# Kernel tuning notes

Hardware: AMD Instinct MI355X
Metric: run time of the kernel (lower is better)

## Reference

```python
import jax, jax.numpy as jnp
import numpy as np
from jax import lax

EPS = 1e-5

def conv2d(x, w, groups=1, pad=0):
    return lax.conv_general_dilated(
        x, w, window_strides=(1, 1), padding=[(pad, pad), (pad, pad)],
        dimension_numbers=('NCHW', 'OIHW', 'NCHW'), feature_group_count=groups)

def setup_inputs() -> dict:
    key = jax.random.key(0)
    ks = jax.random.split(key, 10)
    B, C, H, W = 8, 64, 128, 128
    s = 0.05
    f32 = jnp.float32
    return {
        'x': jax.random.normal(ks[0], (B, C, H, W), f32),
        # key_embed: Conv2d(64,64,3,groups=8,bias=False) -> weight [64, 64/8, 3, 3]
        'w_key': jax.random.normal(ks[1], (64, 8, 3, 3), f32) * s,
        # embed[0]: Conv2d(128,32,1,groups=2,bias=False) -> [32, 128/2, 1, 1]
        'w_e1': jax.random.normal(ks[2], (32, 64, 1, 1), f32) * s,
        # embed[2]: Conv2d(32,72,1,groups=2,bias=True) -> [72, 32/2, 1, 1]
        'w_e2': jax.random.normal(ks[3], (72, 16, 1, 1), f32) * s,
        'b_e2': jax.random.normal(ks[4], (72,), f32) * s,
        # GroupNorm(num_groups=8, num_channels=72) affine params
        'gn_w': jnp.ones((72,), f32),
        'gn_b': jnp.zeros((72,), f32),
        # conv1x1: Conv2d(64,64,1,groups=2,bias=False) -> [64, 32, 1, 1]
        'w_c1': jax.random.normal(ks[5], (64, 32, 1, 1), f32) * s,
        # conv_du: Conv2d(64,4,1,bias=False), Conv2d(4,64,1,bias=False)
        'w_du1': jax.random.normal(ks[6], (4, 64, 1, 1), f32) * s,
        'w_du2': jax.random.normal(ks[7], (64, 4, 1, 1), f32) * s,
    }

def reference(x, w_key, w_e1, w_e2, b_e2, gn_w, gn_b, w_c1, w_du1, w_du2):
    B, C, H, W = x.shape  # C == 64
    KK = 9                # kernel_size^2
    # key embedding: grouped 3x3 conv + ReLU
    k = jax.nn.relu(conv2d(x, w_key, groups=8, pad=1))
    # interleave x and k along channels: view of [B,64,2,H,W] -> [B,128,H,W]
    qk = jnp.stack([x, k], axis=2).reshape(B, 2 * C, H, W)
    # dynamic kernel generation (embed)
    w = jax.nn.relu(conv2d(qk, w_e1, groups=2))
    w = conv2d(w, w_e2, groups=2) + b_e2[None, :, None, None]  # [B,72,H,W]
    # GroupNorm(8, 72): normalize over (channels-in-group, H, W)
    wg = w.reshape(B, 8, 9, H, W)
    m = wg.mean(axis=(2, 3, 4), keepdims=True)
    v = wg.var(axis=(2, 3, 4), keepdims=True)
    w = ((wg - m) * lax.rsqrt(v + EPS)).reshape(B, 72, H, W)
    w = w * gn_w[None, :, None, None] + gn_b[None, :, None, None]
    # per-pixel kernels: [B*2, 4, 9, H, W]
    w = w.reshape(B * 2, 4, KK, H, W)
    # value path
    xv = conv2d(x, w_c1, groups=2).reshape(B * 2, 32, H, W)
    # unfold 3x3 patches with zero padding 1 -> [B*2, 32, 9, H, W]
    xp = jnp.pad(xv, ((0, 0), (0, 0), (1, 1), (1, 1)))
    patches = jnp.stack(
        [xp[:, :, i:i + H, j:j + W] for i in range(3) for j in range(3)], axis=2)
    # share_planes=8: 8 channels share each kernel -> [B*2, 4, 8, 9, H, W]
    patches = patches.reshape(B * 2, 4, 8, KK, H, W)
    out = jnp.einsum('bgckhw,bgkhw->bgchw', patches, w)  # local conv
    out = out.reshape(B, C, H, W)
    # channel attention
    y = out.mean(axis=(2, 3))                 # [B, 64]
    y = jax.nn.relu(y @ w_du1[:, :, 0, 0].T)  # [B, 4]
    y = jax.nn.sigmoid(y @ w_du2[:, :, 0, 0].T)  # [B, 64]
    return out * y[:, :, None, None]
```

## Files before the change

### kernel.cpp

```cpp
#include <hip/hip_runtime.h>
#include <math.h>

#define Hd 128
#define Wd 128
#define HW 16384

__device__ __forceinline__ float wred(float v) {
  #pragma unroll
  for (int o = 32; o > 0; o >>= 1) v += __shfl_down(v, o, 64);
  return v;
}

__global__ __launch_bounds__(256) void k_keyconv(const float* __restrict__ x,
                                                 const float* __restrict__ wkey,
                                                 float* __restrict__ kout) {
  __shared__ float xt[8][34][24];
  const int tid = threadIdx.x;
  const int tx = tid & 15, ty = tid >> 4;
  const int b = blockIdx.z >> 3, g = blockIdx.z & 7;
  const int h0 = blockIdx.y * 32, w0 = blockIdx.x * 16;
  for (int i = tid; i < 8 * 612; i += 256) {
    int ch = i / 612, r = i - ch * 612;
    int yy = r / 18, xx = r - yy * 18;
    int gh = h0 + yy - 1, gw = w0 + xx - 1;
    float v = 0.f;
    if (gh >= 0 && gh < Hd && gw >= 0 && gw < Wd)
      v = x[((long)(b * 64 + g * 8 + ch) << 14) + (gh << 7) + gw];
    xt[ch][yy][xx] = v;
  }
  __syncthreads();
  float acc0[8] = {0.f, 0.f, 0.f, 0.f, 0.f, 0.f, 0.f, 0.f};
  float acc1[8] = {0.f, 0.f, 0.f, 0.f, 0.f, 0.f, 0.f, 0.f};
  const float* wg = wkey + g * 576;
  #pragma unroll
  for (int ich = 0; ich < 8; ++ich) {
    float nb[12];
    #pragma unroll
    for (int rr = 0; rr < 4; ++rr)
      #pragma unroll
      for (int cc = 0; cc < 3; ++cc)
        nb[rr * 3 + cc] = xt[ich][2 * ty + rr][tx + cc];
    #pragma unroll
    for (int oc = 0; oc < 8; ++oc) {
      const float* wr = wg + oc * 72 + ich * 9;
      #pragma unroll
      for (int dy = 0; dy < 3; ++dy)
        #pragma unroll
        for (int dx = 0; dx < 3; ++dx) {
          float wv = wr[dy * 3 + dx];
          acc0[oc] += wv * nb[dy * 3 + dx];
          acc1[oc] += wv * nb[(dy + 1) * 3 + dx];
        }
    }
  }
  const int h = h0 + 2 * ty, w = w0 + tx;
  #pragma unroll
  for (int oc = 0; oc < 8; ++oc) {
    const long base = ((long)(b * 64 + g * 8 + oc) << 14);
    kout[base + (h << 7) + w] = fmaxf(acc0[oc], 0.f);
    kout[base + ((h + 1) << 7) + w] = fmaxf(acc1[oc], 0.f);
  }
}

__global__ __launch_bounds__(128) void k_embed(const float* __restrict__ x,
                                               float* __restrict__ kxv,
                                               const float* __restrict__ we1,
                                               const float* __restrict__ we2,
                                               const float* __restrict__ be2,
                                               const float* __restrict__ wc1,
                                               float* __restrict__ wpre,
                                               float* __restrict__ spart) {
  const int tid = threadIdx.x;
  const int p = blockIdx.x * 128 + tid;
  const int b = blockIdx.y;
  const int s = blockIdx.z;
  float xc[32], kc[32];
  #pragma unroll
  for (int j = 0; j < 32; ++j) {
    xc[j] = x[((long)(b * 64 + 32 * s + j) << 14) + p];
    kc[j] = kxv[((long)(b * 64 + 32 * s + j) << 14) + p];
  }
  #pragma unroll 4
  for (int o = 0; o < 32; ++o) {
    const float* wr = wc1 + (32 * s + o) * 32;
    float a = 0.f;
    #pragma unroll
    for (int j = 0; j < 32; ++j) a += wr[j] * xc[j];
    kxv[((long)(b * 64 + 32 * s + o) << 14) + p] = a;
  }
  float w1a[16];
  #pragma unroll
  for (int o = 0; o < 16; ++o) {
    const float* wr = we1 + (16 * s + o) * 64;
    float a = 0.f;
    #pragma unroll
    for (int j = 0; j < 32; ++j) a += wr[2 * j] * xc[j] + wr[2 * j + 1] * kc[j];
    w1a[o] = fmaxf(a, 0.f);
  }
  const int row = blockIdx.x * 2 + (tid >> 6);
  #pragma unroll
  for (int gl = 0; gl < 4; ++gl) {
    float lgs = 0.f, lgq = 0.f;
    #pragma unroll
    for (int kk = 0; kk < 9; ++kk) {
      const int oc2 = 36 * s + gl * 9 + kk;
      const float* wr = we2 + oc2 * 16;
      float a = be2[oc2];
      #pragma unroll
      for (int ic = 0; ic < 16; ++ic) a += wr[ic] * w1a[ic];
      wpre[((long)(b * 72 + oc2) << 14) + p] = a;
      lgs += a;
      lgq += a * a;
    }
    float r1 = wred(lgs), r2 = wred(lgq);
    if ((tid & 63) == 0) {
      spart[row * 128 + (b * 8 + 4 * s + gl) * 2 + 0] = r1;
      spart[row * 128 + (b * 8 + 4 * s + gl) * 2 + 1] = r2;
    }
  }
}

__global__ void k_gnstat(const float* __restrict__ spart, float* __restrict__ minv) {
  __shared__ float sred[128];
  const int t = threadIdx.x;
  float a = 0.f;
  #pragma unroll 8
  for (int r = 0; r < 256; ++r) a += spart[r * 128 + t];
  sred[t] = a;
  __syncthreads();
  if (t < 64) {
    const float N = 9.f * (float)HW;
    float s = sred[2 * t], q = sred[2 * t + 1];
    float m = s / N;
    float var = q / N - m * m;
    minv[2 * t] = m;
    minv[2 * t + 1] = rsqrtf(var + 1e-5f);
  }
}

__global__ __launch_bounds__(256) void k_local(const float* __restrict__ kxv,
                                               const float* __restrict__ wpre,
                                               const float* __restrict__ minv,
                                               const float* __restrict__ gnw,
                                               const float* __restrict__ gnb,
                                               float* __restrict__ out,
                                               float* __restrict__ part) {
  __shared__ float xt[8][34][24];
  const int tid = threadIdx.x;
  const int tx = tid & 15, ty = tid >> 4;
  const int z = blockIdx.z;
  const int b2 = z >> 2, g = z & 3;
  const int t = b2 & 1, b = b2 >> 1;
  const int h0 = blockIdx.y * 32, w0 = blockIdx.x * 16;
  for (int i = tid; i < 8 * 612; i += 256) {
    int ch = i / 612, r = i - ch * 612;
    int yy = r / 18, xx = r - yy * 18;
    int gh = h0 + yy - 1, gw = w0 + xx - 1;
    float v = 0.f;
    if (gh >= 0 && gh < Hd && gw >= 0 && gw < Wd)
      v = kxv[((long)(b2 * 32 + g * 8 + ch) << 14) + (gh << 7) + gw];
    xt[ch][yy][xx] = v;
  }
  __syncthreads();
  const int gg = 4 * t + g;
  const float m = minv[(b * 8 + gg) * 2];
  const float inv = minv[(b * 8 + gg) * 2 + 1];
  const int p0 = ((h0 + 2 * ty) << 7) + (w0 + tx);
  const int p1 = p0 + 128;
  float wn0[9], wn1[9];
  #pragma unroll
  for (int kk = 0; kk < 9; ++kk) {
    const int ch72 = 36 * t + 9 * g + kk;
    const long base = ((long)(b * 72 + ch72) << 14);
    const float sc = inv * gnw[ch72], sh = gnb[ch72] - m * inv * gnw[ch72];
    wn0[kk] = wpre[base + p0] * sc + sh;
    wn1[kk] = wpre[base + p1] * sc + sh;
  }
  const int prow = (blockIdx.y * 8 + blockIdx.x) * 4 + (tid >> 6);
  #pragma unroll
  for (int cc = 0; cc < 8; ++cc) {
    float nb[12];
    #pragma unroll
    for (int rr = 0; rr < 4; ++rr)
      #pragma unroll
      for (int ccol = 0; ccol < 3; ++ccol)
        nb[rr * 3 + ccol] = xt[cc][2 * ty + rr][tx + ccol];
    float o0 = 0.f, o1 = 0.f;
    #pragma unroll
    for (int dy = 0; dy < 3; ++dy)
      #pragma unroll
      for (int dx = 0; dx < 3; ++dx) {
        o0 += wn0[dy * 3 + dx] * nb[dy * 3 + dx];
        o1 += wn1[dy * 3 + dx] * nb[(dy + 1) * 3 + dx];
      }
    const int ch512 = b2 * 32 + g * 8 + cc;
    out[((long)ch512 << 14) + p0] = o0;
    out[((long)ch512 << 14) + p1] = o1;
    float os = wred(o0 + o1);
    if ((tid & 63) == 0) part[prow * 512 + ch512] = os;
  }
}

__global__ void k_ca(const float* __restrict__ part, const float* __restrict__ du1,
                     const float* __restrict__ du2, float* __restrict__ ys) {
  __shared__ float sy[8][64];
  __shared__ float sy4[8][4];
  const int tid = threadIdx.x;
  const int b = tid >> 6, c = tid & 63;
  float acc = 0.f;
  #pragma unroll 8
  for (int r = 0; r < 128; ++r) acc += part[r * 512 + tid];
  sy[b][c] = acc * (1.f / (float)HW);
  __syncthreads();
  if (tid < 32) {
    int bb = tid >> 2, j = tid & 3;
    float a = 0.f;
    for (int c2 = 0; c2 < 64; ++c2) a += sy[bb][c2] * du1[j * 64 + c2];
    sy4[bb][j] = fmaxf(a, 0.f);
  }
  __syncthreads();
  float z = 0.f;
  #pragma unroll
  for (int j = 0; j < 4; ++j) z += sy4[b][j] * du2[c * 4 + j];
  ys[tid] = 1.f / (1.f + expf(-z));
}

__global__ __launch_bounds__(256) void k_scale(float* __restrict__ out,
                                               const float* __restrict__ ys) {
  const long i4 = (long)blockIdx.x * 256 + threadIdx.x;
  const long e = i4 * 4;
  const int bc = (int)(e >> 14);
  const float s = ys[bc];
  float4* o = (float4*)out;
  float4 v = o[i4];
  v.x *= s; v.y *= s; v.z *= s; v.w *= s;
  o[i4] = v;
}

extern "C" void kernel_launch(void* const* d_in, const int* in_sizes, int n_in,
                              void* d_out, int out_size, void* d_ws, size_t ws_size,
                              hipStream_t stream) {
  const float* x    = (const float*)d_in[0];
  const float* wkey = (const float*)d_in[1];
  const float* we1  = (const float*)d_in[2];
  const float* we2  = (const float*)d_in[3];
  const float* be2  = (const float*)d_in[4];
  const float* gnw  = (const float*)d_in[5];
  const float* gnb  = (const float*)d_in[6];
  const float* wc1  = (const float*)d_in[7];
  const float* du1  = (const float*)d_in[8];
  const float* du2  = (const float*)d_in[9];
  float* out = (float*)d_out;
  float* ws = (float*)d_ws;

  float* kxv  = ws;
  float* wpre = ws + 8388608;
  float* part = ws + 17825792;
  float* spart = part;
  float* minv = part + 131072;
  float* ys   = minv + 128;

  k_keyconv<<<dim3(8, 4, 64), 256, 0, stream>>>(x, wkey, kxv);
  k_embed<<<dim3(128, 8, 2), 128, 0, stream>>>(x, kxv, we1, we2, be2, wc1, wpre, spart);
  k_gnstat<<<1, 128, 0, stream>>>(spart, minv);
  k_local<<<dim3(8, 4, 64), 256, 0, stream>>>(kxv, wpre, minv, gnw, gnb, out, part);
  k_ca<<<1, 512, 0, stream>>>(part, du1, du2, ys);
  k_scale<<<8192, 256, 0, stream>>>(out, ys);
}
```

Before: 243.1 us.

## Fuse grouped 3x3 key conv into embed kernel, keeping k in registers

Merges the key-embedding 3x3 grouped conv and the embed/value 1x1 convs into one kernel over 16x16 spatial tiles. Each block loads four 8-channel haloed tiles of x into LDS, computes k in registers and takes x from the tile centre. This removes the global write and re-read of the k tensor and one kernel launch. The cost is a grid of only 1024 blocks, higher register pressure, and partial-sum rows remapped to the new tile layout.

Result: slower. 313.7 us (+29.0%).

```diff
diff --git a/kernel.cpp b/kernel.cpp
--- a/kernel.cpp
+++ b/kernel.cpp
@@ -11,74 +11,56 @@
   return v;
 }
 
-__global__ __launch_bounds__(256) void k_keyconv(const float* __restrict__ x,
-                                                 const float* __restrict__ wkey,
-                                                 float* __restrict__ kout) {
-  __shared__ float xt[8][34][24];
-  const int tid = threadIdx.x;
-  const int tx = tid & 15, ty = tid >> 4;
-  const int b = blockIdx.z >> 3, g = blockIdx.z & 7;
-  const int h0 = blockIdx.y * 32, w0 = blockIdx.x * 16;
-  for (int i = tid; i < 8 * 612; i += 256) {
-    int ch = i / 612, r = i - ch * 612;
-    int yy = r / 18, xx = r - yy * 18;
-    int gh = h0 + yy - 1, gw = w0 + xx - 1;
-    float v = 0.f;
-    if (gh >= 0 && gh < Hd && gw >= 0 && gw < Wd)
-      v = x[((long)(b * 64 + g * 8 + ch) << 14) + (gh << 7) + gw];
-    xt[ch][yy][xx] = v;
-  }
-  __syncthreads();
-  float acc0[8] = {0.f, 0.f, 0.f, 0.f, 0.f, 0.f, 0.f, 0.f};
-  float acc1[8] = {0.f, 0.f, 0.f, 0.f, 0.f, 0.f, 0.f, 0.f};
-  const float* wg = wkey + g * 576;
-  #pragma unroll
-  for (int ich = 0; ich < 8; ++ich) {
-    float nb[12];
-    #pragma unroll
-    for (int rr = 0; rr < 4; ++rr)
-      #pragma unroll
-      for (int cc = 0; cc < 3; ++cc)
-        nb[rr * 3 + cc] = xt[ich][2 * ty + rr][tx + cc];
-    #pragma unroll
-    for (int oc = 0; oc < 8; ++oc) {
-      const float* wr = wg + oc * 72 + ich * 9;
-      #pragma unroll
-      for (int dy = 0; dy < 3; ++dy)
-        #pragma unroll
-        for (int dx = 0; dx < 3; ++dx) {
-          float wv = wr[dy * 3 + dx];
-          acc0[oc] += wv * nb[dy * 3 + dx];
-          acc1[oc] += wv * nb[(dy + 1) * 3 + dx];
-        }
-    }
-  }
-  const int h = h0 + 2 * ty, w = w0 + tx;
-  #pragma unroll
-  for (int oc = 0; oc < 8; ++oc) {
-    const long base = ((long)(b * 64 + g * 8 + oc) << 14);
-    kout[base + (h << 7) + w] = fmaxf(acc0[oc], 0.f);
-    kout[base + ((h + 1) << 7) + w] = fmaxf(acc1[oc], 0.f);
-  }
-}
-
-__global__ __launch_bounds__(128) void k_embed(const float* __restrict__ x,
-                                               float* __restrict__ kxv,
+__global__ __launch_bounds__(256) void k_fused(const float* __restrict__ x,
+                                               const float* __restrict__ wkey,
                                                const float* __restrict__ we1,
                                                const float* __restrict__ we2,
                                                const float* __restrict__ be2,
                                                const float* __restrict__ wc1,
+                                               float* __restrict__ xv,
                                                float* __restrict__ wpre,
                                                float* __restrict__ spart) {
+  __shared__ float xt[8][18][24];
   const int tid = threadIdx.x;
-  const int p = blockIdx.x * 128 + tid;
-  const int b = blockIdx.y;
-  const int s = blockIdx.z;
+  const int tx = tid & 15, ty = tid >> 4;
+  const int z = blockIdx.z;
+  const int b = z >> 1, s = z & 1;
+  const int h0 = blockIdx.y * 16, w0 = blockIdx.x * 16;
+  const int p = ((h0 + ty) << 7) + (w0 + tx);
   float xc[32], kc[32];
   #pragma unroll
-  for (int j = 0; j < 32; ++j) {
-    xc[j] = x[((long)(b * 64 + 32 * s + j) << 14) + p];
-    kc[j] = kxv[((long)(b * 64 + 32 * s + j) << 14) + p];
+  for (int g = 0; g < 4; ++g) {
+    if (g) __syncthreads();
+    for (int i = tid; i < 8 * 324; i += 256) {
+      int ch = i / 324, r = i - ch * 324;
+      int yy = r / 18, xx = r - yy * 18;
+      int gh = h0 + yy - 1, gw = w0 + xx - 1;
+      float v = 0.f;
+      if (gh >= 0 && gh < Hd && gw >= 0 && gw < Wd)
+        v = x[((long)(b * 64 + 32 * s + 8 * g + ch) << 14) + (gh << 7) + gw];
+      xt[ch][yy][xx] = v;
+    }
+    __syncthreads();
+    float acc[8] = {0.f, 0.f, 0.f, 0.f, 0.f, 0.f, 0.f, 0.f};
+    const float* wg = wkey + (32 * s + 8 * g) * 72;
+    #pragma unroll
+    for (int ich = 0; ich < 8; ++ich) {
+      float nb[9];
+      #pragma unroll
+      for (int dy = 0; dy < 3; ++dy)
+        #pragma unroll
+        for (int dx = 0; dx < 3; ++dx)
+          nb[dy * 3 + dx] = xt[ich][ty + dy][tx + dx];
+      xc[8 * g + ich] = nb[4];
+      #pragma unroll
+      for (int oc = 0; oc < 8; ++oc) {
+        const float* wr = wg + oc * 72 + ich * 9;
+        #pragma unroll
+        for (int t = 0; t < 9; ++t) acc[oc] += wr[t] * nb[t];
+      }
+    }
+    #pragma unroll
+    for (int oc = 0; oc < 8; ++oc) kc[8 * g + oc] = fmaxf(acc[oc], 0.f);
   }
   #pragma unroll 4
   for (int o = 0; o < 32; ++o) {
@@ -86,7 +68,7 @@
     float a = 0.f;
     #pragma unroll
     for (int j = 0; j < 32; ++j) a += wr[j] * xc[j];
-    kxv[((long)(b * 64 + 32 * s + o) << 14) + p] = a;
+    xv[((long)(b * 64 + 32 * s + o) << 14) + p] = a;
   }
   float w1a[16];
   #pragma unroll
@@ -97,7 +79,7 @@
     for (int j = 0; j < 32; ++j) a += wr[2 * j] * xc[j] + wr[2 * j + 1] * kc[j];
     w1a[o] = fmaxf(a, 0.f);
   }
-  const int row = blockIdx.x * 2 + (tid >> 6);
+  const int row = (blockIdx.y * 8 + blockIdx.x) * 4 + (tid >> 6);
   #pragma unroll
   for (int gl = 0; gl < 4; ++gl) {
     float lgs = 0.f, lgq = 0.f;
@@ -138,7 +120,7 @@
   }
 }
 
-__global__ __launch_bounds__(256) void k_local(const float* __restrict__ kxv,
+__global__ __launch_bounds__(256) void k_local(const float* __restrict__ xv,
                                                const float* __restrict__ wpre,
                                                const float* __restrict__ minv,
                                                const float* __restrict__ gnw,
@@ -158,7 +140,7 @@
     int gh = h0 + yy - 1, gw = w0 + xx - 1;
     float v = 0.f;
     if (gh >= 0 && gh < Hd && gw >= 0 && gw < Wd)
-      v = kxv[((long)(b2 * 32 + g * 8 + ch) << 14) + (gh << 7) + gw];
+      v = xv[((long)(b2 * 32 + g * 8 + ch) << 14) + (gh << 7) + gw];
     xt[ch][yy][xx] = v;
   }
   __syncthreads();
@@ -253,17 +235,17 @@
   float* out = (float*)d_out;
   float* ws = (float*)d_ws;
 
-  float* kxv  = ws;
+  float* xv   = ws;
   float* wpre = ws + 8388608;
   float* part = ws + 17825792;
   float* spart = part;
   float* minv = part + 131072;
   float* ys   = minv + 128;
 
-  k_keyconv<<<dim3(8, 4, 64), 256, 0, stream>>>(x, wkey, kxv);
-  k_embed<<<dim3(128, 8, 2), 128, 0, stream>>>(x, kxv, we1, we2, be2, wc1, wpre, spart);
+  k_fused<<<dim3(8, 8, 16), 256, 0, stream>>>(x, wkey, we1, we2, be2, wc1,
+                                              xv, wpre, spart);
   k_gnstat<<<1, 128, 0, stream>>>(spart, minv);
-  k_local<<<dim3(8, 4, 64), 256, 0, stream>>>(kxv, wpre, minv, gnw, gnb, out, part);
+  k_local<<<dim3(8, 4, 64), 256, 0, stream>>>(xv, wpre, minv, gnw, gnb, out, part);
   k_ca<<<1, 512, 0, stream>>>(part, du1, du2, ys);
   k_scale<<<8192, 256, 0, stream>>>(out, ys);
 }
```
